# Optimization experiments

Measured on AMD Instinct MI355X. Metric: run time of the kernel, lower is better.

## Reference

```python
import jax, jax.numpy as jnp
import numpy as np

B, S, D = 4, 2048, 1024
H = 8
HD = D // H          # head_dim = 128
SCALE = 1.0 / np.sqrt(HD)


def setup_inputs() -> dict:
    key = jax.random.key(0)
    ks = jax.random.split(key, 9)
    def lin_w(k):
        return jax.random.normal(k, (D, D), dtype=jnp.float32) * (1.0 / np.sqrt(D))
    return {
        "hidden_states": jax.random.normal(ks[0], (B, S, D), dtype=jnp.float32),
        "Wq": lin_w(ks[1]), "bq": jax.random.normal(ks[2], (D,), dtype=jnp.float32) * 0.02,
        "Wk": lin_w(ks[3]), "bk": jax.random.normal(ks[4], (D,), dtype=jnp.float32) * 0.02,
        "Wv": lin_w(ks[5]), "bv": jax.random.normal(ks[6], (D,), dtype=jnp.float32) * 0.02,
        "Wo": lin_w(ks[7]), "bo": jax.random.normal(ks[8], (D,), dtype=jnp.float32) * 0.02,
    }


def reference(hidden_states, Wq, bq, Wk, bk, Wv, bv, Wo, bo):
    b, s, _ = hidden_states.shape
    # Linear projections (torch nn.Linear: x @ W.T + b; here W stored as (D, D) acting as W.T)
    Q = hidden_states @ Wq + bq
    K = hidden_states @ Wk + bk
    V = hidden_states @ Wv + bv
    # (b, h, s, hd)
    Q = Q.reshape(b, s, H, HD).transpose(0, 2, 1, 3)
    K = K.reshape(b, s, H, HD).transpose(0, 2, 1, 3)
    V = V.reshape(b, s, H, HD).transpose(0, 2, 1, 3)
    # Quaternion inner product sum_quat Re(k* \otimes q) == plain dot product over head_dim:
    # conjugation negates (x,y,z) and the Hamilton real part w1w2 - x1x2 - y1y2 - z1z2
    # re-negates them, yielding wK wQ + xK xQ + yK yQ + zK zQ per quaternion.
    scores = jnp.einsum("bhqd,bhkd->bhqk", Q, K) * SCALE
    attn = jax.nn.softmax(scores, axis=-1)
    out = jnp.einsum("bhqk,bhkd->bhqd", attn, V)
    out = out.transpose(0, 2, 1, 3).reshape(b, s, D)
    return out @ Wo + bo
```

## Files before the change

kernel.cpp:

```cpp
#include <hip/hip_runtime.h>

typedef _Float16 h8 __attribute__((ext_vector_type(8)));
typedef float fx4 __attribute__((ext_vector_type(4)));

#define D_ 1024
#define S_ 2048
#define H_ 8
#define HD_ 128
static constexpr float SCALE = 0.0883883476483184405f;
static constexpr float LOG2E = 1.44269504088896f;
static constexpr float M0C = 5.0f * 1.44269504088896f;

typedef __attribute__((address_space(3))) void lds_void_t;
typedef __attribute__((address_space(1))) void g_void_t;

__device__ __forceinline__ void gl_lds16(const void* g, void* l) {
  __builtin_amdgcn_global_load_lds((const g_void_t*)(uintptr_t)g,
                                   (lds_void_t*)(uintptr_t)l, 16, 0, 0);
}

__device__ __forceinline__ float fast_exp2(float x) {
#if __has_builtin(__builtin_amdgcn_exp2f)
  return __builtin_amdgcn_exp2f(x);
#else
  return __expf(x * 0.6931471805599453f);
#endif
}

__global__ void cast_f16_kernel(const float* __restrict__ x, _Float16* __restrict__ y, int n8) {
  int i = blockIdx.x * blockDim.x + threadIdx.x;
  if (i >= n8) return;
  float4 v0 = ((const float4*)x)[2 * i];
  float4 v1 = ((const float4*)x)[2 * i + 1];
  h8 o = { (_Float16)v0.x, (_Float16)v0.y, (_Float16)v0.z, (_Float16)v0.w,
           (_Float16)v1.x, (_Float16)v1.y, (_Float16)v1.z, (_Float16)v1.w };
  ((h8*)y)[i] = o;
}

__global__ void transpose_cast_w4(const float* __restrict__ W0, const float* __restrict__ W1,
                                  const float* __restrict__ W2, const float* __restrict__ W3,
                                  _Float16* __restrict__ Wt) {
  __shared__ float tile[32][33];
  const float* W = (blockIdx.z == 0) ? W0 : (blockIdx.z == 1) ? W1 : (blockIdx.z == 2) ? W2 : W3;
  _Float16* dst = Wt + (size_t)blockIdx.z * D_ * D_;
  int bx = blockIdx.x * 32, by = blockIdx.y * 32;
  int tx = threadIdx.x, ty = threadIdx.y;
  for (int i = ty; i < 32; i += 8)
    tile[i][tx] = W[(by + i) * D_ + bx + tx];
  __syncthreads();
  for (int i = ty; i < 32; i += 8)
    dst[(bx + i) * D_ + by + tx] = (_Float16)tile[tx][i];
}

__global__ void transpose_v(const _Float16* __restrict__ Vh, _Float16* __restrict__ Vt) {
  __shared__ _Float16 tile[32][33];
  int s0 = blockIdx.x * 32, d0 = blockIdx.y * 32;
  int bh = blockIdx.z;
  int b = bh >> 3, h = bh & 7;
  int tx = threadIdx.x, ty = threadIdx.y;
  for (int i = ty; i < 32; i += 8)
    tile[i][tx] = Vh[(b * S_ + s0 + i) * D_ + h * HD_ + d0 + tx];
  __syncthreads();
  for (int i = ty; i < 32; i += 8)
    Vt[(bh * HD_ + d0 + i) * S_ + s0 + tx] = tile[tx][i];
}

template <typename OutT>
__device__ __forceinline__ void gemm_body(const _Float16* __restrict__ A,
                                          const _Float16* __restrict__ Bt,
                                          const float* __restrict__ bias,
                                          OutT* __restrict__ C, int m0, int n0) {
  constexpr int K = 1024, N = 1024;
  __shared__ __align__(16) _Float16 As[128 * 64];
  __shared__ __align__(16) _Float16 Bs[128 * 64];
  int tid = threadIdx.x;
  int lane = tid & 63, w = tid >> 6;
  int wr = w >> 1, wc = w & 1;
  int l16 = lane & 15, quad = lane >> 4;
  fx4 acc[4][4] = {};
  for (int k0 = 0; k0 < K; k0 += 64) {
#pragma unroll
    for (int it = 0; it < 4; ++it) {
      int s = it * 256 + tid;
      int row = s >> 3, gc = (s & 7) ^ (row & 7);
      gl_lds16(&A[(m0 + row) * K + k0 + gc * 8], &As[s * 8]);
      gl_lds16(&Bt[(n0 + row) * K + k0 + gc * 8], &Bs[s * 8]);
    }
    __syncthreads();
#pragma unroll
    for (int kk = 0; kk < 2; ++kk) {
      h8 a[4], b[4];
#pragma unroll
      for (int i = 0; i < 4; ++i) {
        int row = wr * 64 + i * 16 + l16;
        a[i] = *(const h8*)&As[(row * 8 + ((kk * 4 + quad) ^ (row & 7))) * 8];
      }
#pragma unroll
      for (int j = 0; j < 4; ++j) {
        int row = wc * 64 + j * 16 + l16;
        b[j] = *(const h8*)&Bs[(row * 8 + ((kk * 4 + quad) ^ (row & 7))) * 8];
      }
#pragma unroll
      for (int i = 0; i < 4; ++i)
#pragma unroll
        for (int j = 0; j < 4; ++j)
          acc[i][j] = __builtin_amdgcn_mfma_f32_16x16x32_f16(a[i], b[j], acc[i][j], 0, 0, 0);
    }
    __syncthreads();
  }
#pragma unroll
  for (int i = 0; i < 4; ++i) {
    int row = m0 + wr * 64 + i * 16 + quad * 4;
#pragma unroll
    for (int j = 0; j < 4; ++j) {
      int col = n0 + wc * 64 + j * 16 + l16;
      float bv_ = bias[col];
#pragma unroll
      for (int r = 0; r < 4; ++r)
        C[(row + r) * N + col] = (OutT)(acc[i][j][r] + bv_);
    }
  }
}

__global__ __launch_bounds__(256) void gemm_qkv(const _Float16* __restrict__ A,
                                                const _Float16* __restrict__ Wt,
                                                const float* __restrict__ bq,
                                                const float* __restrict__ bk,
                                                const float* __restrict__ bv,
                                                _Float16* __restrict__ QKV) {
  int z = blockIdx.z;
  const float* bias = (z == 0) ? bq : ((z == 1) ? bk : bv);
  gemm_body<_Float16>(A, Wt + z * (D_ * D_), bias, QKV + z * (S_ * 4 * D_),
                      blockIdx.y * 128, blockIdx.x * 128);
}

__global__ __launch_bounds__(256) void gemm_out(const _Float16* __restrict__ A,
                                                const _Float16* __restrict__ Wt,
                                                const float* __restrict__ bias,
                                                float* __restrict__ C) {
  gemm_body<float>(A, Wt, bias, C, blockIdx.y * 128, blockIdx.x * 128);
}

__global__ __launch_bounds__(256, 2) void attn_kernel(const _Float16* __restrict__ Qh,
                                                      const _Float16* __restrict__ Kh,
                                                      const _Float16* __restrict__ Vt,
                                                      _Float16* __restrict__ Oh) {
  __shared__ __align__(16) _Float16 Ks[2][64 * 128];
  __shared__ __align__(16) _Float16 Vs[2][128 * 64];
  __shared__ __align__(16) _Float16 Ps[4 * 32 * 64];
  const int tid = threadIdx.x;
  const int lane = tid & 63, w = tid >> 6;
  const int l16 = lane & 15, quad = lane >> 4;

  const int lin = blockIdx.y * gridDim.x + blockIdx.x;
  const int xcd = lin & 7, idx = lin >> 3;
  const int bh = (idx >> 4) * 8 + xcd;
  const int qblk = idx & 15;
  const int b = bh >> 3, h = bh & 7;
  const int q0 = qblk * 128 + w * 32;

  const _Float16* Qp = Qh + (size_t)(b * S_ + q0) * D_ + h * HD_;
  const _Float16* Kp = Kh + (size_t)(b * S_) * D_ + h * HD_;
  const _Float16* Vp = Vt + (size_t)bh * HD_ * S_;
  _Float16* Pw = &Ps[w * 32 * 64];

  int kOff[4], vOff[4], ldsOff[4];
#pragma unroll
  for (int it = 0; it < 4; ++it) {
    int s = it * 256 + tid;
    int rowK = s >> 4, gcK = (s & 15) ^ (rowK & 7);
    kOff[it] = rowK * D_ + gcK * 8;
    int rowV = s >> 3, gcV = (s & 7) ^ (rowV & 7);
    vOff[it] = rowV * S_ + gcV * 8;
    ldsOff[it] = s * 8;
  }

  h8 aq[2][4];
#pragma unroll
  for (int mi = 0; mi < 2; ++mi)
#pragma unroll
    for (int kk = 0; kk < 4; ++kk) {
      h8 v = *(const h8*)&Qp[(mi * 16 + l16) * D_ + kk * 32 + quad * 8];
      aq[mi][kk] = v * (_Float16)(SCALE * LOG2E);
    }

  h8 ones_b;
  {
    _Float16 o1 = (l16 == 0) ? (_Float16)1.0f : (_Float16)0.0f;
    ones_b = (h8){o1, o1, o1, o1, o1, o1, o1, o1};
  }

  fx4 o[2][8] = {};
  fx4 lacc[2] = {};

#pragma unroll
  for (int it = 0; it < 4; ++it)
    gl_lds16(Kp + kOff[it], &Ks[0][ldsOff[it]]);

  for (int t = 0; t < 32; ++t) {
    const int kt = t * 64;
    const int cb = t & 1;
    __syncthreads();

    if (t < 31) {
#pragma unroll
      for (int it = 0; it < 4; ++it)
        gl_lds16(Kp + (kt + 64) * D_ + kOff[it], &Ks[cb ^ 1][ldsOff[it]]);
    }
#pragma unroll
    for (int it = 0; it < 4; ++it)
      gl_lds16(Vp + kt + vOff[it], &Vs[cb][ldsOff[it]]);

    fx4 s_[2][4];
#pragma unroll
    for (int mi = 0; mi < 2; ++mi)
#pragma unroll
      for (int j = 0; j < 4; ++j) s_[mi][j] = (fx4){-M0C, -M0C, -M0C, -M0C};
#pragma unroll
    for (int j = 0; j < 4; ++j) {
      int row = j * 16 + l16;
      h8 bk[4];
#pragma unroll
      for (int kk = 0; kk < 4; ++kk)
        bk[kk] = *(const h8*)&Ks[cb][(row * 16 + ((kk * 4 + quad) ^ (row & 7))) * 8];
#pragma unroll
      for (int kk = 0; kk < 4; ++kk) {
        s_[0][j] = __builtin_amdgcn_mfma_f32_16x16x32_f16(aq[0][kk], bk[kk], s_[0][j], 0, 0, 0);
        s_[1][j] = __builtin_amdgcn_mfma_f32_16x16x32_f16(aq[1][kk], bk[kk], s_[1][j], 0, 0, 0);
      }
    }

    if (t > 0) {
      h8 ap[2][2];
#pragma unroll
      for (int mi = 0; mi < 2; ++mi)
#pragma unroll
        for (int kk = 0; kk < 2; ++kk) {
          int row = mi * 16 + l16;
          ap[mi][kk] = *(const h8*)&Pw[row * 64 + (((kk * 4 + quad) + row) & 7) * 8];
        }
#pragma unroll
      for (int jd = 0; jd < 8; ++jd) {
        int row = jd * 16 + l16;
#pragma unroll
        for (int kk = 0; kk < 2; ++kk) {
          h8 bv = *(const h8*)&Vs[cb ^ 1][(row * 8 + ((kk * 4 + quad) ^ (row & 7))) * 8];
          o[0][jd] = __builtin_amdgcn_mfma_f32_16x16x32_f16(ap[0][kk], bv, o[0][jd], 0, 0, 0);
          o[1][jd] = __builtin_amdgcn_mfma_f32_16x16x32_f16(ap[1][kk], bv, o[1][jd], 0, 0, 0);
        }
      }
#pragma unroll
      for (int kk = 0; kk < 2; ++kk) {
        lacc[0] = __builtin_amdgcn_mfma_f32_16x16x32_f16(ap[0][kk], ones_b, lacc[0], 0, 0, 0);
        lacc[1] = __builtin_amdgcn_mfma_f32_16x16x32_f16(ap[1][kk], ones_b, lacc[1], 0, 0, 0);
      }
    }

#pragma unroll
    for (int mi = 0; mi < 2; ++mi)
#pragma unroll
      for (int r = 0; r < 4; ++r) {
        int row = mi * 16 + quad * 4 + r;
#pragma unroll
        for (int j = 0; j < 4; ++j) {
          float p = fast_exp2(s_[mi][j][r]);
          int c = j * 2 + (l16 >> 3);
          Pw[row * 64 + ((c + row) & 7) * 8 + (l16 & 7)] = (_Float16)p;
        }
      }
  }

  __syncthreads();

  {
    h8 ap[2][2];
#pragma unroll
    for (int mi = 0; mi < 2; ++mi)
#pragma unroll
      for (int kk = 0; kk < 2; ++kk) {
        int row = mi * 16 + l16;
        ap[mi][kk] = *(const h8*)&Pw[row * 64 + (((kk * 4 + quad) + row) & 7) * 8];
      }
#pragma unroll
    for (int jd = 0; jd < 8; ++jd) {
      int row = jd * 16 + l16;
#pragma unroll
      for (int kk = 0; kk < 2; ++kk) {
        h8 bv = *(const h8*)&Vs[1][(row * 8 + ((kk * 4 + quad) ^ (row & 7))) * 8];
        o[0][jd] = __builtin_amdgcn_mfma_f32_16x16x32_f16(ap[0][kk], bv, o[0][jd], 0, 0, 0);
        o[1][jd] = __builtin_amdgcn_mfma_f32_16x16x32_f16(ap[1][kk], bv, o[1][jd], 0, 0, 0);
      }
    }
#pragma unroll
    for (int kk = 0; kk < 2; ++kk) {
      lacc[0] = __builtin_amdgcn_mfma_f32_16x16x32_f16(ap[0][kk], ones_b, lacc[0], 0, 0, 0);
      lacc[1] = __builtin_amdgcn_mfma_f32_16x16x32_f16(ap[1][kk], ones_b, lacc[1], 0, 0, 0);
    }
  }

#pragma unroll
  for (int mi = 0; mi < 2; ++mi)
#pragma unroll
    for (int r = 0; r < 4; ++r) {
      float lsum = __shfl(lacc[mi][r], lane & 48);
      float inv = 1.0f / lsum;
      int row = q0 + mi * 16 + quad * 4 + r;
      _Float16* op = Oh + (size_t)(b * S_ + row) * D_ + h * HD_;
#pragma unroll
      for (int jd = 0; jd < 8; ++jd)
        op[jd * 16 + l16] = (_Float16)(o[mi][jd][r] * inv);
    }
}

extern "C" void kernel_launch(void* const* d_in, const int* in_sizes, int n_in,
                              void* d_out, int out_size, void* d_ws, size_t ws_size,
                              hipStream_t stream) {
  const float* hs = (const float*)d_in[0];
  const float* Wq = (const float*)d_in[1];
  const float* bq = (const float*)d_in[2];
  const float* Wk = (const float*)d_in[3];
  const float* bk = (const float*)d_in[4];
  const float* Wv = (const float*)d_in[5];
  const float* bv = (const float*)d_in[6];
  const float* Wo = (const float*)d_in[7];
  const float* bo = (const float*)d_in[8];
  float* out = (float*)d_out;

  const int MD = S_ * 4 * D_;
  const int WD = D_ * D_;
  _Float16* ws = (_Float16*)d_ws;
  _Float16* hs_h = ws;
  _Float16* WtQ = hs_h + MD;
  _Float16* WtO = WtQ + 3 * WD;
  _Float16* QKVh = WtO + WD;
  _Float16* Vt = QKVh + 3 * MD;
  _Float16* Oh = Vt + MD;

  dim3 tb(32, 8);
  cast_f16_kernel<<<MD / 8 / 256, 256, 0, stream>>>(hs, hs_h, MD / 8);
  transpose_cast_w4<<<dim3(32, 32, 4), tb, 0, stream>>>(Wq, Wk, Wv, Wo, WtQ);

  gemm_qkv<<<dim3(8, 64, 3), 256, 0, stream>>>(hs_h, WtQ, bq, bk, bv, QKVh);
  transpose_v<<<dim3(S_ / 32, HD_ / 32, 32), tb, 0, stream>>>(QKVh + 2 * MD, Vt);
  attn_kernel<<<dim3(S_ / 128, 32), 256, 0, stream>>>(QKVh, QKVh + MD, Vt, Oh);
  gemm_out<<<dim3(8, 64), 256, 0, stream>>>(Oh, WtO, bo, out);
}
```

Measured before the change: 297.4 us.

## Fuse prep kernels and compute transposed scores to drop ones-MFMA row sums

The hidden-state cast and the weight transpose-cast are merged into one launch, which removes one kernel launch. In attention, the score MFMA now computes K·Q^T (swapped operands), so each lane holds four consecutive keys for one query. That layout lets the softmax row sum be accumulated in scalar registers, replacing the extra ones-vector MFMAs, and lets P be written to LDS as packed 4-wide halves instead of scalar stores. Row sums are reduced with shuffles at the end, and the P swizzle is changed to match the new write pattern.

```diff
diff --git a/kernel.cpp b/kernel.cpp
--- a/kernel.cpp
+++ b/kernel.cpp
@@ -1,6 +1,7 @@
 #include <hip/hip_runtime.h>
 
 typedef _Float16 h8 __attribute__((ext_vector_type(8)));
+typedef _Float16 h4 __attribute__((ext_vector_type(4)));
 typedef float fx4 __attribute__((ext_vector_type(4)));
 
 #define D_ 1024
@@ -27,24 +28,27 @@
 #endif
 }
 
-__global__ void cast_f16_kernel(const float* __restrict__ x, _Float16* __restrict__ y, int n8) {
-  int i = blockIdx.x * blockDim.x + threadIdx.x;
-  if (i >= n8) return;
-  float4 v0 = ((const float4*)x)[2 * i];
-  float4 v1 = ((const float4*)x)[2 * i + 1];
-  h8 o = { (_Float16)v0.x, (_Float16)v0.y, (_Float16)v0.z, (_Float16)v0.w,
-           (_Float16)v1.x, (_Float16)v1.y, (_Float16)v1.z, (_Float16)v1.w };
-  ((h8*)y)[i] = o;
-}
-
-__global__ void transpose_cast_w4(const float* __restrict__ W0, const float* __restrict__ W1,
-                                  const float* __restrict__ W2, const float* __restrict__ W3,
-                                  _Float16* __restrict__ Wt) {
+__global__ void prep_kernel(const float* __restrict__ hs, _Float16* __restrict__ hs_h,
+                            const float* __restrict__ W0, const float* __restrict__ W1,
+                            const float* __restrict__ W2, const float* __restrict__ W3,
+                            _Float16* __restrict__ Wt) {
+  int bid = blockIdx.x, tid = threadIdx.x;
+  if (bid < 4096) {
+    int i = bid * 256 + tid;
+    float4 v0 = ((const float4*)hs)[2 * i];
+    float4 v1 = ((const float4*)hs)[2 * i + 1];
+    h8 o = { (_Float16)v0.x, (_Float16)v0.y, (_Float16)v0.z, (_Float16)v0.w,
+             (_Float16)v1.x, (_Float16)v1.y, (_Float16)v1.z, (_Float16)v1.w };
+    ((h8*)hs_h)[i] = o;
+    return;
+  }
   __shared__ float tile[32][33];
-  const float* W = (blockIdx.z == 0) ? W0 : (blockIdx.z == 1) ? W1 : (blockIdx.z == 2) ? W2 : W3;
-  _Float16* dst = Wt + (size_t)blockIdx.z * D_ * D_;
-  int bx = blockIdx.x * 32, by = blockIdx.y * 32;
-  int tx = threadIdx.x, ty = threadIdx.y;
+  int zz = bid - 4096;
+  int wz = zz >> 10, rem = zz & 1023;
+  const float* W = (wz == 0) ? W0 : (wz == 1) ? W1 : (wz == 2) ? W2 : W3;
+  _Float16* dst = Wt + (size_t)wz * D_ * D_;
+  int bx = (rem & 31) * 32, by = (rem >> 5) * 32;
+  int tx = tid & 31, ty = tid >> 5;
   for (int i = ty; i < 32; i += 8)
     tile[i][tx] = W[(by + i) * D_ + bx + tx];
   __syncthreads();
@@ -177,21 +181,18 @@
 
   h8 aq[2][4];
 #pragma unroll
-  for (int mi = 0; mi < 2; ++mi)
-#pragma unroll
-    for (int kk = 0; kk < 4; ++kk) {
-      h8 v = *(const h8*)&Qp[(mi * 16 + l16) * D_ + kk * 32 + quad * 8];
-      aq[mi][kk] = v * (_Float16)(SCALE * LOG2E);
-    }
-
-  h8 ones_b;
-  {
-    _Float16 o1 = (l16 == 0) ? (_Float16)1.0f : (_Float16)0.0f;
-    ones_b = (h8){o1, o1, o1, o1, o1, o1, o1, o1};
-  }
+  for (int nt = 0; nt < 2; ++nt)
+#pragma unroll
+    for (int kf = 0; kf < 4; ++kf) {
+      h8 v = *(const h8*)&Qp[(nt * 16 + l16) * D_ + kf * 32 + quad * 8];
+      aq[nt][kf] = v * (_Float16)(SCALE * LOG2E);
+    }
 
   fx4 o[2][8] = {};
-  fx4 lacc[2] = {};
+  float lp[2] = {0.f, 0.f};
+
+  const int pq = l16;
+  const int pswz = (pq & 7) + (pq >> 3);
 
 #pragma unroll
   for (int it = 0; it < 4; ++it)
@@ -211,22 +212,22 @@
     for (int it = 0; it < 4; ++it)
       gl_lds16(Vp + kt + vOff[it], &Vs[cb][ldsOff[it]]);
 
-    fx4 s_[2][4];
-#pragma unroll
-    for (int mi = 0; mi < 2; ++mi)
-#pragma unroll
-      for (int j = 0; j < 4; ++j) s_[mi][j] = (fx4){-M0C, -M0C, -M0C, -M0C};
-#pragma unroll
-    for (int j = 0; j < 4; ++j) {
-      int row = j * 16 + l16;
-      h8 bk[4];
-#pragma unroll
-      for (int kk = 0; kk < 4; ++kk)
-        bk[kk] = *(const h8*)&Ks[cb][(row * 16 + ((kk * 4 + quad) ^ (row & 7))) * 8];
-#pragma unroll
-      for (int kk = 0; kk < 4; ++kk) {
-        s_[0][j] = __builtin_amdgcn_mfma_f32_16x16x32_f16(aq[0][kk], bk[kk], s_[0][j], 0, 0, 0);
-        s_[1][j] = __builtin_amdgcn_mfma_f32_16x16x32_f16(aq[1][kk], bk[kk], s_[1][j], 0, 0, 0);
+    fx4 st[4][2];
+#pragma unroll
+    for (int mt = 0; mt < 4; ++mt)
+#pragma unroll
+      for (int nt = 0; nt < 2; ++nt) st[mt][nt] = (fx4){-M0C, -M0C, -M0C, -M0C};
+#pragma unroll
+    for (int mt = 0; mt < 4; ++mt) {
+      int row = mt * 16 + l16;
+      h8 ak[4];
+#pragma unroll
+      for (int kf = 0; kf < 4; ++kf)
+        ak[kf] = *(const h8*)&Ks[cb][(row * 16 + ((kf * 4 + quad) ^ (row & 7))) * 8];
+#pragma unroll
+      for (int kf = 0; kf < 4; ++kf) {
+        st[mt][0] = __builtin_amdgcn_mfma_f32_16x16x32_f16(ak[kf], aq[0][kf], st[mt][0], 0, 0, 0);
+        st[mt][1] = __builtin_amdgcn_mfma_f32_16x16x32_f16(ak[kf], aq[1][kf], st[mt][1], 0, 0, 0);
       }
     }
 
@@ -235,38 +236,37 @@
 #pragma unroll
       for (int mi = 0; mi < 2; ++mi)
 #pragma unroll
-        for (int kk = 0; kk < 2; ++kk) {
-          int row = mi * 16 + l16;
-          ap[mi][kk] = *(const h8*)&Pw[row * 64 + (((kk * 4 + quad) + row) & 7) * 8];
+        for (int kc = 0; kc < 2; ++kc) {
+          int q = mi * 16 + l16;
+          int cp = ((kc * 4 + quad) + (q & 7) + (q >> 3)) & 7;
+          ap[mi][kc] = *(const h8*)&Pw[q * 64 + cp * 8];
         }
 #pragma unroll
-      for (int jd = 0; jd < 8; ++jd) {
-        int row = jd * 16 + l16;
-#pragma unroll
-        for (int kk = 0; kk < 2; ++kk) {
-          h8 bv = *(const h8*)&Vs[cb ^ 1][(row * 8 + ((kk * 4 + quad) ^ (row & 7))) * 8];
-          o[0][jd] = __builtin_amdgcn_mfma_f32_16x16x32_f16(ap[0][kk], bv, o[0][jd], 0, 0, 0);
-          o[1][jd] = __builtin_amdgcn_mfma_f32_16x16x32_f16(ap[1][kk], bv, o[1][jd], 0, 0, 0);
+      for (int nt = 0; nt < 8; ++nt) {
+        int rowd = nt * 16 + l16;
+#pragma unroll
+        for (int kc = 0; kc < 2; ++kc) {
+          h8 bv = *(const h8*)&Vs[cb ^ 1][(rowd * 8 + ((kc * 4 + quad) ^ (rowd & 7))) * 8];
+          o[0][nt] = __builtin_amdgcn_mfma_f32_16x16x32_f16(ap[0][kc], bv, o[0][nt], 0, 0, 0);
+          o[1][nt] = __builtin_amdgcn_mfma_f32_16x16x32_f16(ap[1][kc], bv, o[1][nt], 0, 0, 0);
         }
       }
-#pragma unroll
-      for (int kk = 0; kk < 2; ++kk) {
-        lacc[0] = __builtin_amdgcn_mfma_f32_16x16x32_f16(ap[0][kk], ones_b, lacc[0], 0, 0, 0);
-        lacc[1] = __builtin_amdgcn_mfma_f32_16x16x32_f16(ap[1][kk], ones_b, lacc[1], 0, 0, 0);
-      }
-    }
-
-#pragma unroll
-    for (int mi = 0; mi < 2; ++mi)
-#pragma unroll
-      for (int r = 0; r < 4; ++r) {
-        int row = mi * 16 + quad * 4 + r;
-#pragma unroll
-        for (int j = 0; j < 4; ++j) {
-          float p = fast_exp2(s_[mi][j][r]);
-          int c = j * 2 + (l16 >> 3);
-          Pw[row * 64 + ((c + row) & 7) * 8 + (l16 & 7)] = (_Float16)p;
-        }
+    }
+
+#pragma unroll
+    for (int mt = 0; mt < 4; ++mt)
+#pragma unroll
+      for (int nt = 0; nt < 2; ++nt) {
+        float p0 = fast_exp2(st[mt][nt][0]);
+        float p1 = fast_exp2(st[mt][nt][1]);
+        float p2 = fast_exp2(st[mt][nt][2]);
+        float p3 = fast_exp2(st[mt][nt][3]);
+        lp[nt] += (p0 + p1) + (p2 + p3);
+        h4 pk = { (_Float16)p0, (_Float16)p1, (_Float16)p2, (_Float16)p3 };
+        int c = 2 * mt + (quad >> 1);
+        int cp = (c + pswz + 2 * nt) & 7;
+        int off = (16 * nt + pq) * 64 + cp * 8 + 4 * (quad & 1);
+        *(h4*)&Pw[off] = pk;
       }
   }
 
@@ -277,38 +277,41 @@
 #pragma unroll
     for (int mi = 0; mi < 2; ++mi)
 #pragma unroll
-      for (int kk = 0; kk < 2; ++kk) {
-        int row = mi * 16 + l16;
-        ap[mi][kk] = *(const h8*)&Pw[row * 64 + (((kk * 4 + quad) + row) & 7) * 8];
-      }
-#pragma unroll
-    for (int jd = 0; jd < 8; ++jd) {
-      int row = jd * 16 + l16;
-#pragma unroll
-      for (int kk = 0; kk < 2; ++kk) {
-        h8 bv = *(const h8*)&Vs[1][(row * 8 + ((kk * 4 + quad) ^ (row & 7))) * 8];
-        o[0][jd] = __builtin_amdgcn_mfma_f32_16x16x32_f16(ap[0][kk], bv, o[0][jd], 0, 0, 0);
-        o[1][jd] = __builtin_amdgcn_mfma_f32_16x16x32_f16(ap[1][kk], bv, o[1][jd], 0, 0, 0);
-      }
-    }
-#pragma unroll
-    for (int kk = 0; kk < 2; ++kk) {
-      lacc[0] = __builtin_amdgcn_mfma_f32_16x16x32_f16(ap[0][kk], ones_b, lacc[0], 0, 0, 0);
-      lacc[1] = __builtin_amdgcn_mfma_f32_16x16x32_f16(ap[1][kk], ones_b, lacc[1], 0, 0, 0);
-    }
-  }
-
+      for (int kc = 0; kc < 2; ++kc) {
+        int q = mi * 16 + l16;
+        int cp = ((kc * 4 + quad) + (q & 7) + (q >> 3)) & 7;
+        ap[mi][kc] = *(const h8*)&Pw[q * 64 + cp * 8];
+      }
+#pragma unroll
+    for (int nt = 0; nt < 8; ++nt) {
+      int rowd = nt * 16 + l16;
+#pragma unroll
+      for (int kc = 0; kc < 2; ++kc) {
+        h8 bv = *(const h8*)&Vs[1][(rowd * 8 + ((kc * 4 + quad) ^ (rowd & 7))) * 8];
+        o[0][nt] = __builtin_amdgcn_mfma_f32_16x16x32_f16(ap[0][kc], bv, o[0][nt], 0, 0, 0);
+        o[1][nt] = __builtin_amdgcn_mfma_f32_16x16x32_f16(ap[1][kc], bv, o[1][nt], 0, 0, 0);
+      }
+    }
+  }
+
+#pragma unroll
+  for (int nt = 0; nt < 2; ++nt) {
+    float v = lp[nt];
+    v += __shfl_xor(v, 16);
+    v += __shfl_xor(v, 32);
+    lp[nt] = v;
+  }
 #pragma unroll
   for (int mi = 0; mi < 2; ++mi)
 #pragma unroll
     for (int r = 0; r < 4; ++r) {
-      float lsum = __shfl(lacc[mi][r], lane & 48);
+      float lsum = __shfl(lp[mi], quad * 4 + r);
       float inv = 1.0f / lsum;
       int row = q0 + mi * 16 + quad * 4 + r;
       _Float16* op = Oh + (size_t)(b * S_ + row) * D_ + h * HD_;
 #pragma unroll
-      for (int jd = 0; jd < 8; ++jd)
-        op[jd * 16 + l16] = (_Float16)(o[mi][jd][r] * inv);
+      for (int nt = 0; nt < 8; ++nt)
+        op[nt * 16 + l16] = (_Float16)(o[mi][nt][r] * inv);
     }
 }
 
@@ -336,12 +339,9 @@
   _Float16* Vt = QKVh + 3 * MD;
   _Float16* Oh = Vt + MD;
 
-  dim3 tb(32, 8);
-  cast_f16_kernel<<<MD / 8 / 256, 256, 0, stream>>>(hs, hs_h, MD / 8);
-  transpose_cast_w4<<<dim3(32, 32, 4), tb, 0, stream>>>(Wq, Wk, Wv, Wo, WtQ);
-
+  prep_kernel<<<8192, 256, 0, stream>>>(hs, hs_h, Wq, Wk, Wv, Wo, WtQ);
   gemm_qkv<<<dim3(8, 64, 3), 256, 0, stream>>>(hs_h, WtQ, bq, bk, bv, QKVh);
-  transpose_v<<<dim3(S_ / 32, HD_ / 32, 32), tb, 0, stream>>>(QKVh + 2 * MD, Vt);
+  transpose_v<<<dim3(S_ / 32, HD_ / 32, 32), dim3(32, 8), 0, stream>>>(QKVh + 2 * MD, Vt);
   attn_kernel<<<dim3(S_ / 128, 32), 256, 0, stream>>>(QKVh, QKVh + MD, Vt, Oh);
   gemm_out<<<dim3(8, 64), 256, 0, stream>>>(Oh, WtO, bo, out);
 }
```

Result: faster. 286.8 us (-3.6%).
